# Kernel tuning notes

Hardware: AMD Instinct MI355X
Metric: run time of the kernel (lower is better)

Reference implementation:

```python
import jax, jax.numpy as jnp
import numpy as np

NEG = -1e10  # matches the -10000000000.0 boundary padding in the torch code


def nw_forward(theta, A):
    """Needleman-Wunsch forward DP with softmax (logsumexp) operator.

    theta: (B, N, M) match potentials; A: (B,) gap penalty.
    Returns Vt: (B,) terminal alignment scores.
    Recursion: V[i,j] = theta[i-1,j-1] + logsumexp(A+V[i-1,j], V[i-1,j-1], A+V[i,j-1]).
    Implemented as scan over rows (i) with an inner scan over columns (j),
    which honors the sequential DP dependencies without Python loops.
    """
    B, N, M = theta.shape
    dtype = theta.dtype
    # V[0, :] row: V[0,0]=0, V[0,j]=NEG for j>=1
    row0 = jnp.full((B, M + 1), NEG, dtype).at[:, 0].set(0.0)

    def row_step(prev_row, th_row):
        # prev_row: (B, M+1) = V[i-1, 0..M]; th_row: (B, M) = theta[:, i-1, :]
        v_up = prev_row[:, 1:]     # V[i-1, j],   j = 1..M
        v_diag = prev_row[:, :-1]  # V[i-1, j-1], j = 1..M

        def col_step(v_left, inp):
            th_j, vu, vd = inp  # each (B,)
            # order (x, m, y) = (A+up, diag, A+left), matching torch stack(v1,v2,v3)
            v = jnp.stack([A + vu, vd, A + v_left], axis=-1)  # (B, 3)
            v_new = th_j + jax.nn.logsumexp(v, axis=-1)
            return v_new, v_new

        xs = (th_row.T, v_up.T, v_diag.T)  # leading axis M
        v_init = jnp.full((B,), NEG, dtype)  # V[i, 0]
        _, row_vals = jax.lax.scan(col_step, v_init, xs)  # (M, B)
        new_row = jnp.concatenate(
            [jnp.full((B, 1), NEG, dtype), row_vals.T], axis=1)  # (B, M+1)
        return new_row, None

    last_row, _ = jax.lax.scan(row_step, row0, jnp.moveaxis(theta, 1, 0))
    return last_row[:, M]  # Vt = V[:, N, M]


def setup_inputs() -> dict:
    key = jax.random.key(0)
    k1, k2 = jax.random.split(key)
    B, N, M = 32, 512, 512
    theta = jax.random.normal(k1, (B, N, M), dtype=jnp.float32)
    A = jax.random.normal(k2, (B,), dtype=jnp.float32)
    return {"theta": theta, "A": A}


def reference(theta, A):
    return nw_forward(theta, A)
```

## Files before the change

kernel.cpp:

```cpp
#include <hip/hip_runtime.h>
#include <math.h>

#define NEGV  -10000000000.0f
#define LOG2E 1.44269504088896340736f
#define LN2F  0.69314718055994530942f

typedef float f4 __attribute__((ext_vector_type(4)));

constexpr int CS   = 16;
constexpr int ROWS = 80;
constexpr int WL   = 17;
constexpr int CHW  = ROWS * WL;

__global__ __launch_bounds__(512, 2) void nw_kernel(
    const float* __restrict__ theta, const float* __restrict__ A,
    float* __restrict__ out, int N, int M)
{
    __shared__ float thS[8 * 2 * CHW];
    __shared__ f4    bndS4[9 * 2 * 4];
    float* bndS = (float*)bndS4;

    const int tid = threadIdx.x;
    const int w   = tid >> 6;
    const int l   = tid & 63;
    const int j   = tid;
    const int b   = blockIdx.x;
    const int NW  = blockDim.x >> 6;

    if (tid < 9 * 2 * 16) bndS[tid] = NEGV;

    const float a2 = A[b] * LOG2E;
    const float* __restrict__ thb = theta + (size_t)b * N * M;
    const int NM = N * M;

    float v_prev = NEGV;
    float v_diag = (j == 0) ? 0.0f : NEGV;
    float bcarry = NEGV;

    const int T  = N + M - 1;
    const int KC = (T + CS - 1) / CS;

    const int srow = l >> 4;
    const int sq   = l & 15;
    const int lanebase = srow * (M - 1) + 64 * w + 63 + sq;
    const int wrbase0 = (w * 2 + 0) * CHW + srow * WL + sq;
    const int wrbase1 = (w * 2 + 1) * CHW + srow * WL + sq;
    const int rdbase0 = (w * 2 + 0) * CHW + (63 - l) * WL;
    const int rdbase1 = (w * 2 + 1) * CHW + (63 - l) * WL;

    const int wstart = 64 * w;
    const int wend   = 64 * w + 63 + N - 1;

    for (int S = -1; S <= KC - 1 + (NW - 1); ++S) {
        const int cn = S - w + 1;
        const bool st_act = (cn >= 0) && (cn < KC) &&
                            (CS * cn + CS - 1 >= wstart) && (CS * cn <= wend);
        float stg[20];
        if (st_act) {
            const int rb = CS * cn - 64 * w - 63;
            if (rb >= 0 && rb + (ROWS - 1) <= N - 1) {
                const float* p = thb + (size_t)rb * M;
                #pragma unroll
                for (int it = 0; it < 20; ++it) {
                    stg[it] = p[lanebase];
                    p += 4 * (M - 1);
                }
            } else {
                const int rbM = rb * M;
                #pragma unroll
                for (int it = 0; it < 20; ++it) {
                    int off = rbM + lanebase + it * 4 * (M - 1);
                    off = min(max(off, 0), NM - 1);
                    stg[it] = thb[off];
                }
            }
        }

        const int c = S - w;
        const bool valid_c = (c >= 0) && (c < KC);
        const int pc = c & 1;
        float nbcarry = bcarry;
        if (valid_c) nbcarry = bndS[(w * 2 + pc) * 16 + 15];
        const bool cp_act = valid_c &&
                            (CS * c + CS - 1 >= wstart) && (CS * c <= wend);
        if (cp_act) {
            const f4* bsrc = &bndS4[(w * 2 + pc) * 4];
            f4 bq0 = bsrc[0], bq1 = bsrc[1], bq2 = bsrc[2], bq3 = bsrc[3];
            float bv[16] = {bq0.x, bq0.y, bq0.z, bq0.w,  bq1.x, bq1.y, bq1.z, bq1.w,
                            bq2.x, bq2.y, bq2.z, bq2.w,  bq3.x, bq3.y, bq3.z, bq3.w};

            const int rdb = pc ? rdbase1 : rdbase0;
            float th[16];
            #pragma unroll
            for (int k = 0; k < 16; ++k) th[k] = thS[rdb + k * (WL + 1)];

            float res[16];
            const bool full = (CS * c >= 64 * w + 63) &&
                              (CS * c + CS - 1 <= 64 * w + N - 1);
            if (full) {
                #pragma unroll
                for (int k = 0; k < 16; ++k) {
                    float bk = (k == 0) ? bcarry : bv[k - 1];
                    float vl = __int_as_float(__builtin_amdgcn_update_dpp(
                        __float_as_int(bk), __float_as_int(v_prev),
                        0x138 , 0xF, 0xF, false));
                    float x = a2 + v_prev;
                    float z = a2 + vl;
                    float m = fmaxf(fmaxf(x, v_diag), z);
                    float s = __builtin_amdgcn_exp2f(x - m)
                            + __builtin_amdgcn_exp2f(v_diag - m)
                            + __builtin_amdgcn_exp2f(z - m);
                    float v = th[k] + m + __builtin_amdgcn_logf(s);
                    res[k]  = v;
                    v_diag  = vl;
                    v_prev  = v;
                }
            } else {
                const int tmj = CS * c - j;
                #pragma unroll
                for (int k = 0; k < 16; ++k) {
                    float bk = (k == 0) ? bcarry : bv[k - 1];
                    float vl = __int_as_float(__builtin_amdgcn_update_dpp(
                        __float_as_int(bk), __float_as_int(v_prev),
                        0x138, 0xF, 0xF, false));
                    float x = a2 + v_prev;
                    float z = a2 + vl;
                    float m = fmaxf(fmaxf(x, v_diag), z);
                    float s = __builtin_amdgcn_exp2f(x - m)
                            + __builtin_amdgcn_exp2f(v_diag - m)
                            + __builtin_amdgcn_exp2f(z - m);
                    float v = th[k] + m + __builtin_amdgcn_logf(s);
                    int dt  = tmj + k;
                    float vn = ((unsigned)dt < (unsigned)N) ? v
                                                            : (dt < 0 ? NEGV : v_prev);
                    res[k]  = vn;
                    v_diag  = vl;
                    v_prev  = vn;
                }
            }
            if (l == 63) {
                f4* dst = &bndS4[((w + 1) * 2 + pc) * 4];
                dst[0] = (f4){res[0],  res[1],  res[2],  res[3]};
                dst[1] = (f4){res[4],  res[5],  res[6],  res[7]};
                dst[2] = (f4){res[8],  res[9],  res[10], res[11]};
                dst[3] = (f4){res[12], res[13], res[14], res[15]};
            }
        }
        bcarry = nbcarry;

        if (st_act) {
            const int wb = (cn & 1) ? wrbase1 : wrbase0;
            #pragma unroll
            for (int it = 0; it < 20; ++it)
                thS[wb + it * 4 * WL] = stg[it] * LOG2E;
        }
        __syncthreads();
    }

    if (j == M - 1) out[b] = v_prev * LN2F;
}

extern "C" void kernel_launch(void* const* d_in, const int* in_sizes, int n_in,
                              void* d_out, int out_size, void* d_ws, size_t ws_size,
                              hipStream_t stream) {
    const float* theta = (const float*)d_in[0];
    const float* A     = (const float*)d_in[1];
    float* out = (float*)d_out;

    const int B  = in_sizes[1];
    const int NM = in_sizes[0] / B;
    int N = 1;
    while (N * N < NM) N <<= 1;
    const int M = NM / N;

    hipLaunchKernelGGL(nw_kernel, dim3(B), dim3(M), 0, stream,
                       theta, A, out, N, M);
}
```

Baseline: 213.6 us.

## Replace block-wide barriers with per-chunk LDS flags between wavefronts

Each wavefront now walks only its own active chunk range. It waits on per-chunk LDS flags, written with release and read with acquire, for the boundary values from the previous wavefront, instead of all wavefronts stepping in lockstep with __syncthreads each chunk. Boundary storage grows to one slot per chunk, so producers never overwrite data a consumer has not yet read. Theta staging stays double-buffered per wave and relies only on s_waitcnt lgkmcnt. This removes the barrier and idle iterations outside each wave's range. The cost is spin-wait polling with s_sleep, plus a possible ordering hazard if the intra-wave LDS staging depends on visibility across lanes.

```diff
diff --git a/kernel.cpp b/kernel.cpp
--- a/kernel.cpp
+++ b/kernel.cpp
@@ -7,18 +7,19 @@
 
 typedef float f4 __attribute__((ext_vector_type(4)));
 
-constexpr int CS   = 16;
-constexpr int ROWS = 80;
-constexpr int WL   = 17;
-constexpr int CHW  = ROWS * WL;
+constexpr int CS    = 16;
+constexpr int ROWS  = 80;
+constexpr int WL    = 17;
+constexpr int CHW   = ROWS * WL;
+constexpr int KCMAX = 64;
 
 __global__ __launch_bounds__(512, 2) void nw_kernel(
     const float* __restrict__ theta, const float* __restrict__ A,
     float* __restrict__ out, int N, int M)
 {
     __shared__ float thS[8 * 2 * CHW];
-    __shared__ f4    bndS4[9 * 2 * 4];
-    float* bndS = (float*)bndS4;
+    __shared__ float bndD[9 * KCMAX * 16];
+    __shared__ int   flg[9 * KCMAX];
 
     const int tid = threadIdx.x;
     const int w   = tid >> 6;
@@ -27,18 +28,19 @@
     const int b   = blockIdx.x;
     const int NW  = blockDim.x >> 6;
 
-    if (tid < 9 * 2 * 16) bndS[tid] = NEGV;
+    for (int i = tid; i < 9 * KCMAX; i += blockDim.x) flg[i] = 0;
+    __syncthreads();
 
     const float a2 = A[b] * LOG2E;
     const float* __restrict__ thb = theta + (size_t)b * N * M;
     const int NM = N * M;
 
-    float v_prev = NEGV;
-    float v_diag = (j == 0) ? 0.0f : NEGV;
-    float bcarry = NEGV;
-
     const int T  = N + M - 1;
     const int KC = (T + CS - 1) / CS;
+    const int wstart = 64 * w;
+    const int wend   = 64 * w + 63 + N - 1;
+    const int ca = wstart / CS;
+    const int cb = min(KC - 1, wend / CS);
 
     const int srow = l >> 4;
     const int sq   = l & 15;
@@ -48,113 +50,133 @@
     const int rdbase0 = (w * 2 + 0) * CHW + (63 - l) * WL;
     const int rdbase1 = (w * 2 + 1) * CHW + (63 - l) * WL;
 
-    const int wstart = 64 * w;
-    const int wend   = 64 * w + 63 + N - 1;
-
-    for (int S = -1; S <= KC - 1 + (NW - 1); ++S) {
-        const int cn = S - w + 1;
-        const bool st_act = (cn >= 0) && (cn < KC) &&
-                            (CS * cn + CS - 1 >= wstart) && (CS * cn <= wend);
-        float stg[20];
-        if (st_act) {
-            const int rb = CS * cn - 64 * w - 63;
-            if (rb >= 0 && rb + (ROWS - 1) <= N - 1) {
-                const float* p = thb + (size_t)rb * M;
-                #pragma unroll
-                for (int it = 0; it < 20; ++it) {
-                    stg[it] = p[lanebase];
-                    p += 4 * (M - 1);
-                }
-            } else {
-                const int rbM = rb * M;
-                #pragma unroll
-                for (int it = 0; it < 20; ++it) {
-                    int off = rbM + lanebase + it * 4 * (M - 1);
-                    off = min(max(off, 0), NM - 1);
-                    stg[it] = thb[off];
-                }
+    auto stage_load = [&](int cn, float* stg) {
+        const int rb = CS * cn - 64 * w - 63;
+        if (rb >= 0 && rb + (ROWS - 1) <= N - 1) {
+            const float* p = thb + (size_t)rb * M;
+            #pragma unroll
+            for (int it = 0; it < 20; ++it) { stg[it] = p[lanebase]; p += 4 * (M - 1); }
+        } else {
+            const int rbM = rb * M;
+            #pragma unroll
+            for (int it = 0; it < 20; ++it) {
+                int off = rbM + lanebase + it * 4 * (M - 1);
+                off = min(max(off, 0), NM - 1);
+                stg[it] = thb[off];
             }
         }
-
-        const int c = S - w;
-        const bool valid_c = (c >= 0) && (c < KC);
-        const int pc = c & 1;
-        float nbcarry = bcarry;
-        if (valid_c) nbcarry = bndS[(w * 2 + pc) * 16 + 15];
-        const bool cp_act = valid_c &&
-                            (CS * c + CS - 1 >= wstart) && (CS * c <= wend);
-        if (cp_act) {
-            const f4* bsrc = &bndS4[(w * 2 + pc) * 4];
-            f4 bq0 = bsrc[0], bq1 = bsrc[1], bq2 = bsrc[2], bq3 = bsrc[3];
-            float bv[16] = {bq0.x, bq0.y, bq0.z, bq0.w,  bq1.x, bq1.y, bq1.z, bq1.w,
-                            bq2.x, bq2.y, bq2.z, bq2.w,  bq3.x, bq3.y, bq3.z, bq3.w};
-
-            const int rdb = pc ? rdbase1 : rdbase0;
-            float th[16];
-            #pragma unroll
-            for (int k = 0; k < 16; ++k) th[k] = thS[rdb + k * (WL + 1)];
-
-            float res[16];
-            const bool full = (CS * c >= 64 * w + 63) &&
-                              (CS * c + CS - 1 <= 64 * w + N - 1);
-            if (full) {
-                #pragma unroll
-                for (int k = 0; k < 16; ++k) {
-                    float bk = (k == 0) ? bcarry : bv[k - 1];
-                    float vl = __int_as_float(__builtin_amdgcn_update_dpp(
-                        __float_as_int(bk), __float_as_int(v_prev),
-                        0x138 , 0xF, 0xF, false));
-                    float x = a2 + v_prev;
-                    float z = a2 + vl;
-                    float m = fmaxf(fmaxf(x, v_diag), z);
-                    float s = __builtin_amdgcn_exp2f(x - m)
-                            + __builtin_amdgcn_exp2f(v_diag - m)
-                            + __builtin_amdgcn_exp2f(z - m);
-                    float v = th[k] + m + __builtin_amdgcn_logf(s);
-                    res[k]  = v;
-                    v_diag  = vl;
-                    v_prev  = v;
-                }
-            } else {
-                const int tmj = CS * c - j;
-                #pragma unroll
-                for (int k = 0; k < 16; ++k) {
-                    float bk = (k == 0) ? bcarry : bv[k - 1];
-                    float vl = __int_as_float(__builtin_amdgcn_update_dpp(
-                        __float_as_int(bk), __float_as_int(v_prev),
-                        0x138, 0xF, 0xF, false));
-                    float x = a2 + v_prev;
-                    float z = a2 + vl;
-                    float m = fmaxf(fmaxf(x, v_diag), z);
-                    float s = __builtin_amdgcn_exp2f(x - m)
-                            + __builtin_amdgcn_exp2f(v_diag - m)
-                            + __builtin_amdgcn_exp2f(z - m);
-                    float v = th[k] + m + __builtin_amdgcn_logf(s);
-                    int dt  = tmj + k;
-                    float vn = ((unsigned)dt < (unsigned)N) ? v
-                                                            : (dt < 0 ? NEGV : v_prev);
-                    res[k]  = vn;
-                    v_diag  = vl;
-                    v_prev  = vn;
-                }
+    };
+    auto stage_write = [&](int cn, const float* stg) {
+        const int wb = (cn & 1) ? wrbase1 : wrbase0;
+        #pragma unroll
+        for (int it = 0; it < 20; ++it) thS[wb + it * 4 * WL] = stg[it] * LOG2E;
+    };
+    auto wait_flag = [&](int idx) {
+        if (__atomic_load_n(&flg[idx], __ATOMIC_ACQUIRE) == 0) {
+            do { __builtin_amdgcn_s_sleep(1); }
+            while (__atomic_load_n(&flg[idx], __ATOMIC_ACQUIRE) == 0);
+        }
+    };
+
+    float v_prev = NEGV;
+    float v_diag = (j == 0) ? 0.0f : NEGV;
+    float bcarry = NEGV;
+
+    {
+        float s0[20];
+        stage_load(ca, s0);
+        stage_write(ca, s0);
+        __asm__ volatile("s_waitcnt lgkmcnt(0)" ::: "memory");
+    }
+    if (w > 0) {
+        wait_flag(w * KCMAX + (ca - 1));
+        bcarry = bndD[(w * KCMAX + ca - 1) * 16 + 15];
+    }
+
+    float stg[20];
+    bool have = (ca + 1 <= cb);
+    if (have) stage_load(ca + 1, stg);
+
+    for (int c = ca; c <= cb; ++c) {
+        const int rdb = (c & 1) ? rdbase1 : rdbase0;
+        float th[16];
+        #pragma unroll
+        for (int k = 0; k < 16; ++k) th[k] = thS[rdb + k * (WL + 1)];
+
+        const bool need_bv = (w > 0) && (CS * c <= 64 * w + N - 1);
+        float bv[16];
+        if (need_bv) {
+            wait_flag(w * KCMAX + c);
+            const f4* src = (const f4*)&bndD[(w * KCMAX + c) * 16];
+            f4 q0 = src[0], q1 = src[1], q2 = src[2], q3 = src[3];
+            bv[0]=q0.x; bv[1]=q0.y; bv[2]=q0.z; bv[3]=q0.w;
+            bv[4]=q1.x; bv[5]=q1.y; bv[6]=q1.z; bv[7]=q1.w;
+            bv[8]=q2.x; bv[9]=q2.y; bv[10]=q2.z; bv[11]=q2.w;
+            bv[12]=q3.x; bv[13]=q3.y; bv[14]=q3.z; bv[15]=q3.w;
+        } else {
+            #pragma unroll
+            for (int k = 0; k < 16; ++k) bv[k] = NEGV;
+        }
+
+        float res[16];
+        const bool full = (CS * c >= 64 * w + 63) &&
+                          (CS * c + CS - 1 <= 64 * w + N - 1);
+        if (full) {
+            #pragma unroll
+            for (int k = 0; k < 16; ++k) {
+                float bk = (k == 0) ? bcarry : bv[k - 1];
+                float vl = __int_as_float(__builtin_amdgcn_update_dpp(
+                    __float_as_int(bk), __float_as_int(v_prev),
+                    0x138 , 0xF, 0xF, false));
+                float x = a2 + v_prev;
+                float z = a2 + vl;
+                float m = fmaxf(fmaxf(x, v_diag), z);
+                float s = __builtin_amdgcn_exp2f(x - m)
+                        + __builtin_amdgcn_exp2f(v_diag - m)
+                        + __builtin_amdgcn_exp2f(z - m);
+                float v = th[k] + m + __builtin_amdgcn_logf(s);
+                res[k] = v;
+                v_diag = vl;
+                v_prev = v;
             }
-            if (l == 63) {
-                f4* dst = &bndS4[((w + 1) * 2 + pc) * 4];
-                dst[0] = (f4){res[0],  res[1],  res[2],  res[3]};
-                dst[1] = (f4){res[4],  res[5],  res[6],  res[7]};
-                dst[2] = (f4){res[8],  res[9],  res[10], res[11]};
-                dst[3] = (f4){res[12], res[13], res[14], res[15]};
+        } else {
+            const int tmj = CS * c - j;
+            #pragma unroll
+            for (int k = 0; k < 16; ++k) {
+                float bk = (k == 0) ? bcarry : bv[k - 1];
+                float vl = __int_as_float(__builtin_amdgcn_update_dpp(
+                    __float_as_int(bk), __float_as_int(v_prev),
+                    0x138, 0xF, 0xF, false));
+                float x = a2 + v_prev;
+                float z = a2 + vl;
+                float m = fmaxf(fmaxf(x, v_diag), z);
+                float s = __builtin_amdgcn_exp2f(x - m)
+                        + __builtin_amdgcn_exp2f(v_diag - m)
+                        + __builtin_amdgcn_exp2f(z - m);
+                float v = th[k] + m + __builtin_amdgcn_logf(s);
+                int dt = tmj + k;
+                float vn = ((unsigned)dt < (unsigned)N) ? v
+                                                        : (dt < 0 ? NEGV : v_prev);
+                res[k] = vn;
+                v_diag = vl;
+                v_prev = vn;
             }
         }
-        bcarry = nbcarry;
-
-        if (st_act) {
-            const int wb = (cn & 1) ? wrbase1 : wrbase0;
-            #pragma unroll
-            for (int it = 0; it < 20; ++it)
-                thS[wb + it * 4 * WL] = stg[it] * LOG2E;
-        }
-        __syncthreads();
+
+        if (w < NW - 1 && l == 63) {
+            f4* dst = (f4*)&bndD[((w + 1) * KCMAX + c) * 16];
+            dst[0] = (f4){res[0],  res[1],  res[2],  res[3]};
+            dst[1] = (f4){res[4],  res[5],  res[6],  res[7]};
+            dst[2] = (f4){res[8],  res[9],  res[10], res[11]};
+            dst[3] = (f4){res[12], res[13], res[14], res[15]};
+            __atomic_store_n(&flg[(w + 1) * KCMAX + c], 1, __ATOMIC_RELEASE);
+        }
+        bcarry = bv[15];
+
+        if (have) stage_write(c + 1, stg);
+        have = (c + 2 <= cb);
+        if (have) stage_load(c + 2, stg);
+        __asm__ volatile("s_waitcnt lgkmcnt(0)" ::: "memory");
     }
 
     if (j == M - 1) out[b] = v_prev * LN2F;
```

Result: faster. 182.2 us (-14.7%).
